# Optimization experiments

Hardware: AMD Instinct MI355X
Metric: run time of the kernel (lower is better)

## Reference

```python
import jax, jax.numpy as jnp
import numpy as np

B = 2097152   # batch
Z = 16        # z_dim
K = 64        # num_hidden_nodes


def setup_inputs() -> dict:
    key = jax.random.key(0)
    k1, k2, k3, k4, k5 = jax.random.split(key, 5)
    return {
        "z": jax.random.normal(k1, (B, Z), dtype=jnp.float32),
        "a_0": jax.random.normal(k2, (1,), dtype=jnp.float32),
        "bk": jax.random.normal(k3, (K,), dtype=jnp.float32),
        "ck": jax.random.normal(k4, (K, Z), dtype=jnp.float32),
        "dk": jax.random.normal(k5, (K,), dtype=jnp.float32),
    }


def reference(z, a_0, bk, ck, dk):
    # Vectorized over the batch: y[b] = a_0 + sum_k bk[k] * tanh((ck @ z[b])[k] + dk[k])
    h = jnp.tanh(jnp.einsum("bz,kz->bk", z, ck) + dk)  # [B, K]
    y = a_0 + h @ bk                                     # [B]
    return y[:, None]                                     # [B, 1]
```

## Files before the change

kernel.cpp:

```cpp
#include <hip/hip_runtime.h>
#include <stdint.h>

typedef __attribute__((ext_vector_type(8)))  short  short8;
typedef __attribute__((ext_vector_type(8)))  __bf16 bf16x8;
typedef __attribute__((ext_vector_type(16))) float  floatx16;
typedef __attribute__((ext_vector_type(4)))  float  floatx4;
typedef __attribute__((ext_vector_type(2)))  float  float2v;
typedef __attribute__((ext_vector_type(4)))  uint32_t uint4v;

union Frag { short8 s; bf16x8 v; uint4v d; };
union FU   { float f; uint32_t u; };

__device__ __forceinline__ short f2bf(float f) {
    FU x; x.f = f;
    uint32_t r = x.u + 0x7fffu + ((x.u >> 16) & 1u);
    return (short)(r >> 16);
}

__device__ __forceinline__ uint32_t pack_bf2(float lo, float hi) {
    FU a, b; a.f = lo; b.f = hi;
    return __builtin_amdgcn_perm(b.u + 0x8000u, a.u + 0x8000u, 0x07060302u);
}

__device__ __forceinline__ float fexp2(float x) { return __builtin_amdgcn_exp2f(x); }
__device__ __forceinline__ float frcp(float x)  { return __builtin_amdgcn_rcpf(x); }

__device__ __forceinline__ float2v tpair(float a, float b) {
    float2v t;
    t.x = fexp2(fminf(a, 15.0f));
    t.y = fexp2(fminf(b, 15.0f));
    return t + 1.0f;
}

__global__ __launch_bounds__(256, 7) void mave_kernel(
    const float* __restrict__ z,
    const float* __restrict__ a0,
    const float* __restrict__ bk,
    const float* __restrict__ ck,
    const float* __restrict__ dk,
    float* __restrict__ out,
    int ntiles)
{
    const int lane = threadIdx.x & 63;
    const int m    = lane & 31;
    const int g    = lane >> 5;
    const int widx = threadIdx.x >> 6;
    const float S  = 2.885390081777927f;

    __shared__ __align__(16) float   cinitL[4][2][2][16];
    __shared__ __align__(16) float2v nbL[4][2][2][8];

    const int wid   = (int)((blockIdx.x * blockDim.x + threadIdx.x) >> 6);
    const int tile0 = wid * 2;
    if (tile0 >= ntiles) return;
    const int tlast = ntiles - 1;

    const float* c0 = ck + m * 16 + g * 8;
    floatx4 ckv0 = *(const floatx4*)c0;
    floatx4 ckv1 = *(const floatx4*)(c0 + 4);
    floatx4 ckv2 = *(const floatx4*)(c0 + 512);
    floatx4 ckv3 = *(const floatx4*)(c0 + 516);

    const int tl = lane;
    const int gg = tl >> 5, hh = (tl >> 4) & 1, rr = tl & 15;
    const int nc = (rr & 3) + 8 * (rr >> 2) + 4 * gg + 32 * hh;
    float dkv = dk[nc];
    float bkt = bk[tl];
    const int g2 = tl >> 4, h2 = (tl >> 3) & 1, j2 = tl & 7;
    const int nl = (j2 & 3) + 8 * (j2 >> 2) + 4 * g2 + 32 * h2;
    float bnl = 0.0f, bnh = 0.0f;
    if (tl < 32) { bnl = bk[nl]; bnh = bk[nl + 16]; }
    float a0v = a0[0];

    const float* zp = z + (size_t)m * 16 + g * 8;
    floatx4 zb[2][2];
    #pragma unroll
    for (int i = 0; i < 2; ++i) {
        int ti = tile0 + i; if (ti > tlast) ti = tlast;
        const float* q = zp + (size_t)ti * 512;
        zb[i][0] = *(const floatx4*)q;
        zb[i][1] = *(const floatx4*)(q + 4);
    }

    Frag af[2];
    #pragma unroll
    for (int e = 0; e < 4; ++e) {
        af[0].s[e]     = f2bf(ckv0[e] * S);
        af[0].s[e + 4] = f2bf(ckv1[e] * S);
        af[1].s[e]     = f2bf(ckv2[e] * S);
        af[1].s[e + 4] = f2bf(ckv3[e] * S);
    }

    cinitL[widx][gg][hh][rr] = S * dkv;
    if (tl < 32) {
        float2v nb; nb.x = -2.0f * bnl; nb.y = -2.0f * bnh;
        nbL[widx][g2][h2][j2] = nb;
    }
    float bv = bkt;
    #pragma unroll
    for (int d = 1; d < 64; d <<= 1) bv += __shfl_xor(bv, d, 64);
    const float base = a0v + bv;

    const floatx4* cqg = (const floatx4*)&cinitL[widx][g][0][0];
    const floatx4* nqg = (const floatx4*)&nbL[widx][g][0][0];

    float yv[2];
    #pragma unroll
    for (int i = 0; i < 2; ++i) {
        Frag bfr;
        bfr.d[0] = pack_bf2(zb[i][0].x, zb[i][0].y);
        bfr.d[1] = pack_bf2(zb[i][0].z, zb[i][0].w);
        bfr.d[2] = pack_bf2(zb[i][1].x, zb[i][1].y);
        bfr.d[3] = pack_bf2(zb[i][1].z, zb[i][1].w);

        int zz = 0;
        asm volatile("" : "+v"(zz));
        const floatx4* cq = cqg + zz;
        const floatx4* nq = nqg + zz;

        float ya = 0.0f;
        #pragma unroll
        for (int h = 0; h < 2; ++h) {
            union { floatx16 v; floatx4 q[4]; } C;
            C.q[0] = cq[h * 4 + 0]; C.q[1] = cq[h * 4 + 1];
            C.q[2] = cq[h * 4 + 2]; C.q[3] = cq[h * 4 + 3];
            floatx16 acc = __builtin_amdgcn_mfma_f32_32x32x16_bf16(
                af[h].v, bfr.v, C.v, 0, 0, 0);

            union { floatx4 q; float2v p[2]; } N0, N1, N2, N3;
            N0.q = nq[h * 4 + 0];
            N1.q = nq[h * 4 + 1];
            N2.q = nq[h * 4 + 2];
            N3.q = nq[h * 4 + 3];

            float2v T0 = tpair(acc[0], acc[8]);
            float2v T1 = tpair(acc[1], acc[9]);
            float2v P01 = T0 * T1;
            float2v n01 = N0.p[0] * T1 + N0.p[1] * T0;
            float2v T2 = tpair(acc[2], acc[10]);
            float2v T3 = tpair(acc[3], acc[11]);
            float2v P23 = T2 * T3;
            float2v n23 = N1.p[0] * T3 + N1.p[1] * T2;
            float2v T4 = tpair(acc[4], acc[12]);
            float2v T5 = tpair(acc[5], acc[13]);
            float2v P45 = T4 * T5;
            float2v n45 = N2.p[0] * T5 + N2.p[1] * T4;
            float2v T6 = tpair(acc[6], acc[14]);
            float2v T7 = tpair(acc[7], acc[15]);
            float2v P67 = T6 * T7;
            float2v n67 = N3.p[0] * T7 + N3.p[1] * T6;

            float2v PA = P01 * P23, PB = P45 * P67;
            float2v nA = n01 * P23 + n23 * P01;
            float2v nB = n45 * P67 + n67 * P45;
            float2v P  = PA * PB;
            float2v Num = nA * PB + nB * PA;
            float2v R; R.x = frcp(P.x); R.y = frcp(P.y);
            float2v Yh = Num * R;
            ya += Yh.x + Yh.y;
        }
        yv[i] = ya;
    }

    float ov[2];
    #pragma unroll
    for (int i = 0; i < 2; ++i) ov[i] = __shfl_xor(yv[i], 32, 64);
    if (g == 0) {
        #pragma unroll
        for (int i = 0; i < 2; ++i) {
            int ti = tile0 + i; if (ti > tlast) ti = tlast;
            out[(size_t)ti * 32 + m] = base + yv[i] + ov[i];
        }
    }
}

extern "C" void kernel_launch(void* const* d_in, const int* in_sizes, int n_in,
                              void* d_out, int out_size, void* d_ws, size_t ws_size,
                              hipStream_t stream) {
    const float* z  = (const float*)d_in[0];
    const float* a0 = (const float*)d_in[1];
    const float* bk = (const float*)d_in[2];
    const float* ck = (const float*)d_in[3];
    const float* dk = (const float*)d_in[4];
    float* out = (float*)d_out;

    const int B      = in_sizes[0] / 16;
    const int ntiles = B / 32;

    const int blocks = (ntiles + 7) / 8;
    hipLaunchKernelGGL(mave_kernel, dim3(blocks), dim3(256), 0, stream,
                       z, a0, bk, ck, dk, out, ntiles);
}
```

Measured before the change: 196.5 us.

## Use persistent grid-stride waves with a three-deep z prefetch ring

The kernel now launches at most 2048 blocks, and each wave strides over tiles with grid stride W. It keeps a rotating three-slot register buffer of z loads, so the next tiles' loads are issued while the current tile's MFMA and tanh math runs. This removes per-block setup (ck fragments, LDS constants, bias reduction) being redone for every two tiles, and it hides global load latency inside each wave. The cost is more registers, with occupancy lowered to 6 waves per SIMD, and fewer waves in flight overall. Redundant clamped loads at the tail are also added.

```diff
diff --git a/kernel.cpp b/kernel.cpp
--- a/kernel.cpp
+++ b/kernel.cpp
@@ -32,7 +32,83 @@
     return t + 1.0f;
 }
 
-__global__ __launch_bounds__(256, 7) void mave_kernel(
+__device__ __forceinline__ float tile_compute(
+    const Frag (&af)[2], const Frag& bfr,
+    const floatx4* cq, const floatx4* nq)
+{
+    float ya = 0.0f;
+    #pragma unroll
+    for (int h = 0; h < 2; ++h) {
+        union { floatx16 v; floatx4 q[4]; } C;
+        C.q[0] = cq[h * 4 + 0]; C.q[1] = cq[h * 4 + 1];
+        C.q[2] = cq[h * 4 + 2]; C.q[3] = cq[h * 4 + 3];
+        floatx16 acc = __builtin_amdgcn_mfma_f32_32x32x16_bf16(
+            af[h].v, bfr.v, C.v, 0, 0, 0);
+
+        union { floatx4 q; float2v p[2]; } N0, N1, N2, N3;
+        N0.q = nq[h * 4 + 0];
+        N1.q = nq[h * 4 + 1];
+        N2.q = nq[h * 4 + 2];
+        N3.q = nq[h * 4 + 3];
+
+        float2v T0 = tpair(acc[0], acc[8]);
+        float2v T1 = tpair(acc[1], acc[9]);
+        float2v P01 = T0 * T1;
+        float2v n01 = N0.p[0] * T1 + N0.p[1] * T0;
+        float2v T2 = tpair(acc[2], acc[10]);
+        float2v T3 = tpair(acc[3], acc[11]);
+        float2v P23 = T2 * T3;
+        float2v n23 = N1.p[0] * T3 + N1.p[1] * T2;
+        float2v T4 = tpair(acc[4], acc[12]);
+        float2v T5 = tpair(acc[5], acc[13]);
+        float2v P45 = T4 * T5;
+        float2v n45 = N2.p[0] * T5 + N2.p[1] * T4;
+        float2v T6 = tpair(acc[6], acc[14]);
+        float2v T7 = tpair(acc[7], acc[15]);
+        float2v P67 = T6 * T7;
+        float2v n67 = N3.p[0] * T7 + N3.p[1] * T6;
+
+        float2v PA = P01 * P23, PB = P45 * P67;
+        float2v nA = n01 * P23 + n23 * P01;
+        float2v nB = n45 * P67 + n67 * P45;
+        float2v P  = PA * PB;
+        float2v Num = nA * PB + nB * PA;
+        float2v R; R.x = frcp(P.x); R.y = frcp(P.y);
+        float2v Yh = Num * R;
+        ya += Yh.x + Yh.y;
+    }
+    return ya;
+}
+
+template<int S>
+__device__ __forceinline__ void tile_step(
+    floatx4 (&zb)[3][2], int& t, int W, int tlast, const float* zp,
+    const Frag (&af)[2], const floatx4* cqg, const floatx4* nqg,
+    float base, float* __restrict__ out, int m, int g)
+{
+    Frag bfr;
+    bfr.d[0] = pack_bf2(zb[S][0].x, zb[S][0].y);
+    bfr.d[1] = pack_bf2(zb[S][0].z, zb[S][0].w);
+    bfr.d[2] = pack_bf2(zb[S][1].x, zb[S][1].y);
+    bfr.d[3] = pack_bf2(zb[S][1].z, zb[S][1].w);
+
+    {
+        int tn = t + 3 * W; if (tn > tlast) tn = tlast;
+        const float* q = zp + (size_t)tn * 512;
+        zb[S][0] = *(const floatx4*)q;
+        zb[S][1] = *(const floatx4*)(q + 4);
+    }
+
+    int zz = 0;
+    asm volatile("" : "+v"(zz));
+    float ya = tile_compute(af, bfr, cqg + zz, nqg + zz);
+
+    float ov = __shfl_xor(ya, 32, 64);
+    if (g == 0) out[(size_t)t * 32 + m] = base + ya + ov;
+    t += W;
+}
+
+__global__ __launch_bounds__(256, 6) void mave_kernel(
     const float* __restrict__ z,
     const float* __restrict__ a0,
     const float* __restrict__ bk,
@@ -50,10 +126,11 @@
     __shared__ __align__(16) float   cinitL[4][2][2][16];
     __shared__ __align__(16) float2v nbL[4][2][2][8];
 
-    const int wid   = (int)((blockIdx.x * blockDim.x + threadIdx.x) >> 6);
-    const int tile0 = wid * 2;
-    if (tile0 >= ntiles) return;
+    const int W   = (int)(gridDim.x << 2);
+    const int wid = (int)(blockIdx.x * 4 + widx);
+    if (wid >= ntiles) return;
     const int tlast = ntiles - 1;
+    const int iters = (tlast - wid) / W + 1;
 
     const float* c0 = ck + m * 16 + g * 8;
     floatx4 ckv0 = *(const floatx4*)c0;
@@ -73,10 +150,10 @@
     float a0v = a0[0];
 
     const float* zp = z + (size_t)m * 16 + g * 8;
-    floatx4 zb[2][2];
-    #pragma unroll
-    for (int i = 0; i < 2; ++i) {
-        int ti = tile0 + i; if (ti > tlast) ti = tlast;
+    floatx4 zb[3][2];
+    #pragma unroll
+    for (int i = 0; i < 3; ++i) {
+        int ti = wid + i * W; if (ti > tlast) ti = tlast;
         const float* q = zp + (size_t)ti * 512;
         zb[i][0] = *(const floatx4*)q;
         zb[i][1] = *(const floatx4*)(q + 4);
@@ -104,73 +181,15 @@
     const floatx4* cqg = (const floatx4*)&cinitL[widx][g][0][0];
     const floatx4* nqg = (const floatx4*)&nbL[widx][g][0][0];
 
-    float yv[2];
-    #pragma unroll
-    for (int i = 0; i < 2; ++i) {
-        Frag bfr;
-        bfr.d[0] = pack_bf2(zb[i][0].x, zb[i][0].y);
-        bfr.d[1] = pack_bf2(zb[i][0].z, zb[i][0].w);
-        bfr.d[2] = pack_bf2(zb[i][1].x, zb[i][1].y);
-        bfr.d[3] = pack_bf2(zb[i][1].z, zb[i][1].w);
-
-        int zz = 0;
-        asm volatile("" : "+v"(zz));
-        const floatx4* cq = cqg + zz;
-        const floatx4* nq = nqg + zz;
-
-        float ya = 0.0f;
-        #pragma unroll
-        for (int h = 0; h < 2; ++h) {
-            union { floatx16 v; floatx4 q[4]; } C;
-            C.q[0] = cq[h * 4 + 0]; C.q[1] = cq[h * 4 + 1];
-            C.q[2] = cq[h * 4 + 2]; C.q[3] = cq[h * 4 + 3];
-            floatx16 acc = __builtin_amdgcn_mfma_f32_32x32x16_bf16(
-                af[h].v, bfr.v, C.v, 0, 0, 0);
-
-            union { floatx4 q; float2v p[2]; } N0, N1, N2, N3;
-            N0.q = nq[h * 4 + 0];
-            N1.q = nq[h * 4 + 1];
-            N2.q = nq[h * 4 + 2];
-            N3.q = nq[h * 4 + 3];
-
-            float2v T0 = tpair(acc[0], acc[8]);
-            float2v T1 = tpair(acc[1], acc[9]);
-            float2v P01 = T0 * T1;
-            float2v n01 = N0.p[0] * T1 + N0.p[1] * T0;
-            float2v T2 = tpair(acc[2], acc[10]);
-            float2v T3 = tpair(acc[3], acc[11]);
-            float2v P23 = T2 * T3;
-            float2v n23 = N1.p[0] * T3 + N1.p[1] * T2;
-            float2v T4 = tpair(acc[4], acc[12]);
-            float2v T5 = tpair(acc[5], acc[13]);
-            float2v P45 = T4 * T5;
-            float2v n45 = N2.p[0] * T5 + N2.p[1] * T4;
-            float2v T6 = tpair(acc[6], acc[14]);
-            float2v T7 = tpair(acc[7], acc[15]);
-            float2v P67 = T6 * T7;
-            float2v n67 = N3.p[0] * T7 + N3.p[1] * T6;
-
-            float2v PA = P01 * P23, PB = P45 * P67;
-            float2v nA = n01 * P23 + n23 * P01;
-            float2v nB = n45 * P67 + n67 * P45;
-            float2v P  = PA * PB;
-            float2v Num = nA * PB + nB * PA;
-            float2v R; R.x = frcp(P.x); R.y = frcp(P.y);
-            float2v Yh = Num * R;
-            ya += Yh.x + Yh.y;
-        }
-        yv[i] = ya;
-    }
-
-    float ov[2];
-    #pragma unroll
-    for (int i = 0; i < 2; ++i) ov[i] = __shfl_xor(yv[i], 32, 64);
-    if (g == 0) {
-        #pragma unroll
-        for (int i = 0; i < 2; ++i) {
-            int ti = tile0 + i; if (ti > tlast) ti = tlast;
-            out[(size_t)ti * 32 + m] = base + yv[i] + ov[i];
-        }
+    int t   = wid;
+    int rem = iters;
+    for (;;) {
+        tile_step<0>(zb, t, W, tlast, zp, af, cqg, nqg, base, out, m, g);
+        if (--rem == 0) break;
+        tile_step<1>(zb, t, W, tlast, zp, af, cqg, nqg, base, out, m, g);
+        if (--rem == 0) break;
+        tile_step<2>(zb, t, W, tlast, zp, af, cqg, nqg, base, out, m, g);
+        if (--rem == 0) break;
     }
 }
 
@@ -187,7 +206,8 @@
     const int B      = in_sizes[0] / 16;
     const int ntiles = B / 32;
 
-    const int blocks = (ntiles + 7) / 8;
+    int blocks = (ntiles + 3) / 4;
+    if (blocks > 2048) blocks = 2048;
     hipLaunchKernelGGL(mave_kernel, dim3(blocks), dim3(256), 0, stream,
                        z, a0, bk, ck, dk, out, ntiles);
 }
```

Result: slower. 205.6 us (+4.6%).

## Use persistent waves with a global-to-LDS prefetch ring for z tiles

Applied to the files above, without the earlier changes.

Changes the kernel from one-shot waves handling two tiles each to a persistent grid of 768 blocks. Each wave strides over tiles and prefetches z four tiles ahead into a per-wave LDS ring using global_load_lds with explicit vmcnt waits. The dk/bk-derived constants move from LDS into registers, loaded once per wave, and launch bounds drop from 7 to 3 waves per SIMD. The aim is to hide memory latency through explicit software pipelining. The cost is higher register pressure, lower occupancy and the risk that hand-counted vmcnt values mismatch the loads actually in flight.

```diff
diff --git a/kernel.cpp b/kernel.cpp
--- a/kernel.cpp
+++ b/kernel.cpp
@@ -32,7 +32,42 @@
     return t + 1.0f;
 }
 
-__global__ __launch_bounds__(256, 7) void mave_kernel(
+typedef const __attribute__((address_space(1))) void* gas_t;
+typedef __attribute__((address_space(3)))       void* las_t;
+__device__ __forceinline__ void gload16(const void* g, void* l) {
+    __builtin_amdgcn_global_load_lds((gas_t)g, (las_t)l, 16, 0, 0);
+}
+
+__device__ __forceinline__ float half_tanh_reg(const floatx16& acc, const float2v* nb)
+{
+    float2v T0 = tpair(acc[0], acc[8]);
+    float2v T1 = tpair(acc[1], acc[9]);
+    float2v P01 = T0 * T1;
+    float2v n01 = nb[0] * T1 + nb[1] * T0;
+    float2v T2 = tpair(acc[2], acc[10]);
+    float2v T3 = tpair(acc[3], acc[11]);
+    float2v P23 = T2 * T3;
+    float2v n23 = nb[2] * T3 + nb[3] * T2;
+    float2v T4 = tpair(acc[4], acc[12]);
+    float2v T5 = tpair(acc[5], acc[13]);
+    float2v P45 = T4 * T5;
+    float2v n45 = nb[4] * T5 + nb[5] * T4;
+    float2v T6 = tpair(acc[6], acc[14]);
+    float2v T7 = tpair(acc[7], acc[15]);
+    float2v P67 = T6 * T7;
+    float2v n67 = nb[6] * T7 + nb[7] * T6;
+
+    float2v PA = P01 * P23, PB = P45 * P67;
+    float2v nA = n01 * P23 + n23 * P01;
+    float2v nB = n45 * P67 + n67 * P45;
+    float2v P  = PA * PB;
+    float2v Num = nA * PB + nB * PA;
+    float2v R; R.x = frcp(P.x); R.y = frcp(P.y);
+    float2v Yh = Num * R;
+    return Yh.x + Yh.y;
+}
+
+__global__ __launch_bounds__(256, 3) void mave_kernel(
     const float* __restrict__ z,
     const float* __restrict__ a0,
     const float* __restrict__ bk,
@@ -47,41 +82,19 @@
     const int widx = threadIdx.x >> 6;
     const float S  = 2.885390081777927f;
 
-    __shared__ __align__(16) float   cinitL[4][2][2][16];
-    __shared__ __align__(16) float2v nbL[4][2][2][8];
-
-    const int wid   = (int)((blockIdx.x * blockDim.x + threadIdx.x) >> 6);
-    const int tile0 = wid * 2;
-    if (tile0 >= ntiles) return;
+    __shared__ __align__(16) char ring[4][4][2048];
+
+    const int W   = (int)(gridDim.x << 2);
+    const int wid = (int)(blockIdx.x * 4 + widx);
+    if (wid >= ntiles) return;
     const int tlast = ntiles - 1;
+    const int iters = (tlast - wid) / W + 1;
 
     const float* c0 = ck + m * 16 + g * 8;
     floatx4 ckv0 = *(const floatx4*)c0;
     floatx4 ckv1 = *(const floatx4*)(c0 + 4);
     floatx4 ckv2 = *(const floatx4*)(c0 + 512);
     floatx4 ckv3 = *(const floatx4*)(c0 + 516);
-
-    const int tl = lane;
-    const int gg = tl >> 5, hh = (tl >> 4) & 1, rr = tl & 15;
-    const int nc = (rr & 3) + 8 * (rr >> 2) + 4 * gg + 32 * hh;
-    float dkv = dk[nc];
-    float bkt = bk[tl];
-    const int g2 = tl >> 4, h2 = (tl >> 3) & 1, j2 = tl & 7;
-    const int nl = (j2 & 3) + 8 * (j2 >> 2) + 4 * g2 + 32 * h2;
-    float bnl = 0.0f, bnh = 0.0f;
-    if (tl < 32) { bnl = bk[nl]; bnh = bk[nl + 16]; }
-    float a0v = a0[0];
-
-    const float* zp = z + (size_t)m * 16 + g * 8;
-    floatx4 zb[2][2];
-    #pragma unroll
-    for (int i = 0; i < 2; ++i) {
-        int ti = tile0 + i; if (ti > tlast) ti = tlast;
-        const float* q = zp + (size_t)ti * 512;
-        zb[i][0] = *(const floatx4*)q;
-        zb[i][1] = *(const floatx4*)(q + 4);
-    }
-
     Frag af[2];
     #pragma unroll
     for (int e = 0; e < 4; ++e) {
@@ -91,87 +104,81 @@
         af[1].s[e + 4] = f2bf(ckv3[e] * S);
     }
 
-    cinitL[widx][gg][hh][rr] = S * dkv;
-    if (tl < 32) {
-        float2v nb; nb.x = -2.0f * bnl; nb.y = -2.0f * bnh;
-        nbL[widx][g2][h2][j2] = nb;
-    }
+    floatx16 cinit[2];
+    #pragma unroll
+    for (int r = 0; r < 16; ++r) {
+        int n = (r & 3) + 8 * (r >> 2) + 4 * g;
+        cinit[0][r] = S * dk[n];
+        cinit[1][r] = S * dk[n + 32];
+    }
+    float2v nb[2][8];
+    #pragma unroll
+    for (int h = 0; h < 2; ++h)
+        #pragma unroll
+        for (int j = 0; j < 8; ++j) {
+            int nl = (j & 3) + 8 * (j >> 2) + 4 * g + 32 * h;
+            nb[h][j].x = -2.0f * bk[nl];
+            nb[h][j].y = -2.0f * bk[nl + 16];
+        }
+    float bkt = bk[lane];
+    float a0v = a0[0];
+
+    const float* zp = z + (size_t)m * 16 + g * 8;
+    #pragma unroll
+    for (int s = 0; s < 4; ++s) {
+        int ti = wid + s * W; if (ti > tlast) ti = tlast;
+        const float* q = zp + (size_t)ti * 512;
+        gload16(q,     &ring[widx][s][0]);
+        gload16(q + 4, &ring[widx][s][1024]);
+    }
+
     float bv = bkt;
     #pragma unroll
     for (int d = 1; d < 64; d <<= 1) bv += __shfl_xor(bv, d, 64);
     const float base = a0v + bv;
 
-    const floatx4* cqg = (const floatx4*)&cinitL[widx][g][0][0];
-    const floatx4* nqg = (const floatx4*)&nbL[widx][g][0][0];
-
-    float yv[2];
-    #pragma unroll
-    for (int i = 0; i < 2; ++i) {
-        Frag bfr;
-        bfr.d[0] = pack_bf2(zb[i][0].x, zb[i][0].y);
-        bfr.d[1] = pack_bf2(zb[i][0].z, zb[i][0].w);
-        bfr.d[2] = pack_bf2(zb[i][1].x, zb[i][1].y);
-        bfr.d[3] = pack_bf2(zb[i][1].z, zb[i][1].w);
-
-        int zz = 0;
-        asm volatile("" : "+v"(zz));
-        const floatx4* cq = cqg + zz;
-        const floatx4* nq = nqg + zz;
-
-        float ya = 0.0f;
-        #pragma unroll
-        for (int h = 0; h < 2; ++h) {
-            union { floatx16 v; floatx4 q[4]; } C;
-            C.q[0] = cq[h * 4 + 0]; C.q[1] = cq[h * 4 + 1];
-            C.q[2] = cq[h * 4 + 2]; C.q[3] = cq[h * 4 + 3];
-            floatx16 acc = __builtin_amdgcn_mfma_f32_32x32x16_bf16(
-                af[h].v, bfr.v, C.v, 0, 0, 0);
-
-            union { floatx4 q; float2v p[2]; } N0, N1, N2, N3;
-            N0.q = nq[h * 4 + 0];
-            N1.q = nq[h * 4 + 1];
-            N2.q = nq[h * 4 + 2];
-            N3.q = nq[h * 4 + 3];
-
-            float2v T0 = tpair(acc[0], acc[8]);
-            float2v T1 = tpair(acc[1], acc[9]);
-            float2v P01 = T0 * T1;
-            float2v n01 = N0.p[0] * T1 + N0.p[1] * T0;
-            float2v T2 = tpair(acc[2], acc[10]);
-            float2v T3 = tpair(acc[3], acc[11]);
-            float2v P23 = T2 * T3;
-            float2v n23 = N1.p[0] * T3 + N1.p[1] * T2;
-            float2v T4 = tpair(acc[4], acc[12]);
-            float2v T5 = tpair(acc[5], acc[13]);
-            float2v P45 = T4 * T5;
-            float2v n45 = N2.p[0] * T5 + N2.p[1] * T4;
-            float2v T6 = tpair(acc[6], acc[14]);
-            float2v T7 = tpair(acc[7], acc[15]);
-            float2v P67 = T6 * T7;
-            float2v n67 = N3.p[0] * T7 + N3.p[1] * T6;
-
-            float2v PA = P01 * P23, PB = P45 * P67;
-            float2v nA = n01 * P23 + n23 * P01;
-            float2v nB = n45 * P67 + n67 * P45;
-            float2v P  = PA * PB;
-            float2v Num = nA * PB + nB * PA;
-            float2v R; R.x = frcp(P.x); R.y = frcp(P.y);
-            float2v Yh = Num * R;
-            ya += Yh.x + Yh.y;
-        }
-        yv[i] = ya;
-    }
-
-    float ov[2];
-    #pragma unroll
-    for (int i = 0; i < 2; ++i) ov[i] = __shfl_xor(yv[i], 32, 64);
-    if (g == 0) {
-        #pragma unroll
-        for (int i = 0; i < 2; ++i) {
-            int ti = tile0 + i; if (ti > tlast) ti = tlast;
-            out[(size_t)ti * 32 + m] = base + yv[i] + ov[i];
-        }
-    }
+    #define STEP(SLOT, VMN)                                                   \
+    do {                                                                      \
+        asm volatile("s_waitcnt vmcnt(" #VMN ")" ::: "memory");               \
+        __builtin_amdgcn_sched_barrier(0);                                    \
+        const floatx4* sp = (const floatx4*)&ring[widx][SLOT][0];             \
+        floatx4 z0 = sp[lane];         \
+        floatx4 z1 = sp[64 + lane];                                           \
+        Frag bfr;                                                             \
+        bfr.d[0] = pack_bf2(z0.x, z0.y);                                      \
+        bfr.d[1] = pack_bf2(z0.z, z0.w);                                      \
+        bfr.d[2] = pack_bf2(z1.x, z1.y);                                      \
+        bfr.d[3] = pack_bf2(z1.z, z1.w);                                      \
+        float ya = 0.0f;                                                      \
+        _Pragma("unroll")                                                     \
+        for (int h = 0; h < 2; ++h) {                                         \
+            floatx16 acc = __builtin_amdgcn_mfma_f32_32x32x16_bf16(           \
+                af[h].v, bfr.v, cinit[h], 0, 0, 0);                           \
+            ya += half_tanh_reg(acc, nb[h]);                                  \
+        }                                                                     \
+        {                \
+            int tn = t + 4 * W; if (tn > tlast) tn = tlast;                   \
+            const float* q = zp + (size_t)tn * 512;                           \
+            gload16(q,     &ring[widx][SLOT][0]);                             \
+            gload16(q + 4, &ring[widx][SLOT][1024]);                          \
+        }                                                                     \
+        float ov = __shfl_xor(ya, 32, 64);                                    \
+        if (g == 0) out[(size_t)t * 32 + m] = base + ya + ov;                 \
+        t += W;                                                               \
+    } while (0)
+
+    int t = wid, rem = iters;
+    STEP(0, 6); if (--rem == 0) return;
+    STEP(1, 6); if (--rem == 0) return;
+    STEP(2, 6); if (--rem == 0) return;
+    STEP(3, 6); if (--rem == 0) return;
+    for (;;) {
+        STEP(0, 9); if (--rem == 0) break;
+        STEP(1, 9); if (--rem == 0) break;
+        STEP(2, 9); if (--rem == 0) break;
+        STEP(3, 9); if (--rem == 0) break;
+    }
+    #undef STEP
 }
 
 extern "C" void kernel_launch(void* const* d_in, const int* in_sizes, int n_in,
@@ -187,7 +194,8 @@
     const int B      = in_sizes[0] / 16;
     const int ntiles = B / 32;
 
-    const int blocks = (ntiles + 7) / 8;
+    int blocks = (ntiles + 15) / 16;
+    if (blocks > 768) blocks = 768;
     hipLaunchKernelGGL(mave_kernel, dim3(blocks), dim3(256), 0, stream,
                        z, a0, bk, ck, dk, out, ntiles);
 }
```

Measured after the change: 200.8 us. 1.02x slower.
